# Optimization experiments

Measured on AMD Instinct MI355X. Metric: run time of the kernel, lower is better.

Reference implementation:

```python
import jax, jax.numpy as jnp
import numpy as np

N_NODES, N_EDGES, F_DIM, H_DIM = 50000, 800000, 128, 128
BN_EPS = 1e-3  # keras BatchNormalization default epsilon


def setup_inputs() -> dict:
    key = jax.random.key(0)
    k0, k1, k2 = jax.random.split(key, 3)
    edge_pairs = jax.random.randint(k0, (N_EDGES, 2), 0, N_NODES, dtype=jnp.int64 if jax.config.jax_enable_x64 else jnp.int32)
    node_features = jax.random.normal(k1, (N_NODES, F_DIM), dtype=jnp.float32)
    W = jax.random.normal(k2, (F_DIM, H_DIM), dtype=jnp.float32) * (1.0 / np.sqrt(F_DIM))
    b = jnp.zeros((H_DIM,), jnp.float32)
    gamma = jnp.ones((H_DIM,), jnp.float32)
    beta = jnp.zeros((H_DIM,), jnp.float32)
    moving_mean = jnp.zeros((H_DIM,), jnp.float32)
    moving_var = jnp.ones((H_DIM,), jnp.float32)
    return {"edge_pairs": edge_pairs, "node_features": node_features, "W": W, "b": b,
            "gamma": gamma, "beta": beta, "moving_mean": moving_mean, "moving_var": moving_var}


def reference(edge_pairs, node_features, W, b, gamma, beta, moving_mean, moving_var):
    src = edge_pairs[:, 0]
    dst = edge_pairs[:, 1]
    n = node_features.shape[0]

    # linear transform (dropout inactive: training=False)
    t = node_features @ W + b  # [N, H]

    # out-degree by source node
    deg = jax.ops.segment_sum(jnp.ones(src.shape[0], t.dtype), src, num_segments=n)  # [N]
    inv_sqrt_deg = jnp.power(deg, -0.5)  # matches tf.pow(d, -0.5)

    # degree-normalized neighbour messages: d_src^-1/2 * d_dst^-1/2 * t[dst]
    scale = (inv_sqrt_deg[src] * inv_sqrt_deg[dst])[:, None]  # [E,1]
    nb_sum = jax.ops.segment_sum(t[dst] * scale, src, num_segments=n)  # [N, H]

    # source term: segment_mean(deg[src] * t[src]) ; empty segments -> 0 (tf semantics)
    msg = deg[src][:, None] * t[src]  # [E, H]
    seg = jax.ops.segment_sum(msg, src, num_segments=n)  # [N, H]
    src_mean = jnp.where(deg[:, None] > 0, seg / jnp.maximum(deg, 1.0)[:, None], 0.0)

    agg = 0.5 * nb_sum + 0.5 * src_mean

    # batchnorm, inference mode (moving statistics)
    return (agg - moving_mean) * jax.lax.rsqrt(moving_var + BN_EPS) * gamma + beta
```

## Files before the change

kernel.cpp:

```cpp
#include <hip/hip_runtime.h>
#include <math.h>

#define BN_EPS 0.001f
#define CHUNK 2048
#define MAXBUCK 1024

typedef __attribute__((ext_vector_type(8))) short bf16x8;
typedef __attribute__((ext_vector_type(4))) float f32x4;
typedef __attribute__((ext_vector_type(2))) float f32x2;

__device__ inline unsigned bf16rne(float f) {
  unsigned u = __float_as_uint(f);
  return (u + 0x7fffu + ((u >> 16) & 1u)) >> 16;
}

__global__ __launch_bounds__(256) void k_ehist(const int2* __restrict__ ep, int ne,
                                               int nbuck, int* __restrict__ ghist) {
  __shared__ int h[MAXBUCK];
  int c = blockIdx.x, t = threadIdx.x;
  for (int i = t; i < nbuck; i += 256) h[i] = 0;
  __syncthreads();
  int base = c * CHUNK;
  int end = min(base + CHUNK, ne);
  for (int e = base + t; e < end; e += 256) atomicAdd(&h[ep[e].x >> 6], 1);
  __syncthreads();
  int* row = ghist + (size_t)c * nbuck;
  for (int i = t; i < nbuck; i += 256) row[i] = h[i];
}

__global__ __launch_bounds__(512) void k_bscan(int* __restrict__ ghist, int nchunk,
                                               int nbuck, int* __restrict__ btot) {
  __shared__ int s0[512], s1[512];
  int b = blockIdx.x, t = threadIdx.x;
  int v = (t < nchunk) ? ghist[(size_t)t * nbuck + b] : 0;
  s0[t] = v;
  __syncthreads();
  int* src = s0; int* dst = s1;
  for (int off = 1; off < 512; off <<= 1) {
    int x = src[t];
    if (t >= off) x += src[t - off];
    dst[t] = x;
    __syncthreads();
    int* tmp = src; src = dst; dst = tmp;
  }
  if (t < nchunk) ghist[(size_t)t * nbuck + b] = src[t] - v;
  if (t == 0) btot[b] = src[511];
}

__global__ __launch_bounds__(1024) void k_bbase(const int* __restrict__ btot, int nbuck,
                                                int* __restrict__ bbase) {
  __shared__ int s0[1024], s1[1024];
  int t = threadIdx.x;
  int v = (t < nbuck) ? btot[t] : 0;
  s0[t] = v;
  __syncthreads();
  int* src = s0; int* dst = s1;
  for (int off = 1; off < 1024; off <<= 1) {
    int x = src[t];
    if (t >= off) x += src[t - off];
    dst[t] = x;
    __syncthreads();
    int* tmp = src; src = dst; dst = tmp;
  }
  if (t < nbuck) bbase[t] = src[t] - v;
}

__global__ __launch_bounds__(256) void k_ebin(const int2* __restrict__ ep, int ne,
                                              int nbuck, const int* __restrict__ ghist,
                                              const int* __restrict__ bbase,
                                              unsigned* __restrict__ bins) {
  __shared__ int cur[MAXBUCK];
  int c = blockIdx.x, t = threadIdx.x;
  const int* row = ghist + (size_t)c * nbuck;
  for (int i = t; i < nbuck; i += 256) cur[i] = bbase[i] + row[i];
  __syncthreads();
  int base = c * CHUNK;
  int end = min(base + CHUNK, ne);
  for (int e = base + t; e < end; e += 256) {
    int2 p = ep[e];
    int pos = atomicAdd(&cur[p.x >> 6], 1);
    bins[pos] = (unsigned)p.y | ((unsigned)(p.x & 63) << 17);
  }
}

__global__ __launch_bounds__(256) void k_bfinal(const int* __restrict__ bbase,
                                                const int* __restrict__ btot,
                                                const unsigned* __restrict__ bins,
                                                int n, int* __restrict__ deg,
                                                float* __restrict__ isd,
                                                int* __restrict__ offsets,
                                                int* __restrict__ csr_dst) {
  __shared__ int h[64];
  __shared__ int cur[64];
  int bk = blockIdx.x, t = threadIdx.x;
  if (t < 64) h[t] = 0;
  __syncthreads();
  int s = bbase[bk], cnt = btot[bk];
  for (int i = t; i < cnt; i += 256) atomicAdd(&h[bins[s + i] >> 17], 1);
  __syncthreads();
  if (t == 0) {
    int run = s;
    for (int j = 0; j < 64; ++j) { cur[j] = run; run += h[j]; }
  }
  __syncthreads();
  if (t < 64) {
    int node = (bk << 6) + t;
    if (node < n) {
      deg[node] = h[t];
      offsets[node] = cur[t];
      isd[node] = 1.0f / sqrtf((float)h[t]);
    }
  }
  __syncthreads();
  for (int i = t; i < cnt; i += 256) {
    unsigned r = bins[s + i];
    int pos = atomicAdd(&cur[r >> 17], 1);
    csr_dst[pos] = (int)(r & 0x1FFFFu);
  }
}

__global__ __launch_bounds__(256) void k_wsplit(const float* __restrict__ W,
                                                unsigned short* __restrict__ Wh,
                                                unsigned short* __restrict__ Wl) {
  int g = blockIdx.x * 256 + threadIdx.x;
  int frag = g >> 6;
  int lane = g & 63;
  int ct = frag >> 2, ks = frag & 3;
  int col = ct * 16 + (lane & 15);
  int k0 = ks * 32 + (lane >> 4) * 8;
  unsigned short h8[8], l8[8];
#pragma unroll
  for (int j = 0; j < 8; ++j) {
    float x = W[(size_t)(k0 + j) * 128 + col];
    unsigned short h = (unsigned short)(__float_as_uint(x) >> 16);
    float rem = x - __uint_as_float((unsigned)h << 16);
    h8[j] = h;
    l8[j] = (unsigned short)bf16rne(rem);
  }
  *(uint4*)&Wh[(size_t)frag * 512 + lane * 8] = *(uint4*)h8;
  *(uint4*)&Wl[(size_t)frag * 512 + lane * 8] = *(uint4*)l8;
}

__global__ __launch_bounds__(256, 4) void k_gemm(const float* __restrict__ X,
                                                 const unsigned short* __restrict__ Wh,
                                                 const unsigned short* __restrict__ Wl,
                                                 const float* __restrict__ b,
                                                 const float* __restrict__ isd,
                                                 float* __restrict__ T,
                                                 unsigned char* __restrict__ Tb8, int M) {
  int tid = threadIdx.x;
  int wave = tid >> 6, lane = tid & 63;
  int r16 = lane & 15, kq = lane >> 4;
  int ch = wave & 1;
  int rowbase = blockIdx.x * 32 + (wave >> 1) * 16;
  int arow = rowbase + r16;
  bool aok = arow < M;
  const float* xr = X + ((size_t)arow << 7);

  bf16x8 ah[4], al[4];
#pragma unroll
  for (int ks = 0; ks < 4; ++ks) {
    int k0 = ks * 32 + kq * 8;
    float4 v0 = aok ? *(const float4*)(xr + k0) : make_float4(0.f, 0.f, 0.f, 0.f);
    float4 v1 = aok ? *(const float4*)(xr + k0 + 4) : make_float4(0.f, 0.f, 0.f, 0.f);
    float f[8] = {v0.x, v0.y, v0.z, v0.w, v1.x, v1.y, v1.z, v1.w};
    bf16x8 h8, l8;
#pragma unroll
    for (int j = 0; j < 8; ++j) {
      unsigned short h = (unsigned short)(__float_as_uint(f[j]) >> 16);
      float rem = f[j] - __uint_as_float((unsigned)h << 16);
      h8[j] = (short)h;
      l8[j] = (short)bf16rne(rem);
    }
    ah[ks] = h8;
    al[ks] = l8;
  }

  f32x4 acc[4] = {};
#pragma unroll
  for (int ks = 0; ks < 4; ++ks) {
#pragma unroll
    for (int ct = 0; ct < 4; ++ct) {
      int frag = (ch * 4 + ct) * 4 + ks;
      bf16x8 bh = *(const bf16x8*)&Wh[(size_t)frag * 512 + lane * 8];
      bf16x8 bl = *(const bf16x8*)&Wl[(size_t)frag * 512 + lane * 8];
      acc[ct] = __builtin_amdgcn_mfma_f32_16x16x32_bf16(ah[ks], bh, acc[ct], 0, 0, 0);
      acc[ct] = __builtin_amdgcn_mfma_f32_16x16x32_bf16(ah[ks], bl, acc[ct], 0, 0, 0);
      acc[ct] = __builtin_amdgcn_mfma_f32_16x16x32_bf16(al[ks], bh, acc[ct], 0, 0, 0);
    }
  }

  float bias[4];
#pragma unroll
  for (int ct = 0; ct < 4; ++ct) bias[ct] = b[(ch * 4 + ct) * 16 + r16];
  int orow[4];
  float isdr[4];
#pragma unroll
  for (int r = 0; r < 4; ++r) {
    orow[r] = rowbase + kq * 4 + r;
    isdr[r] = (orow[r] < M) ? isd[orow[r]] : 0.f;
  }
#pragma unroll
  for (int ct = 0; ct < 4; ++ct) {
    int col = (ch * 4 + ct) * 16 + r16;
#pragma unroll
    for (int r = 0; r < 4; ++r) {
      float v = acc[ct][r] + bias[ct];
      bool ok = orow[r] < M;
      if (ok) T[((size_t)orow[r] << 7) + col] = v;
      float sv = v * isdr[r];
      float other = __shfl_xor(sv, 1);
      int pk01 = __builtin_amdgcn_cvt_pk_fp8_f32(sv, other, 0, false);
      int pk23 = __shfl_xor(pk01, 2);
      if (ok && (r16 & 3) == 0) {
        unsigned dword = ((unsigned)pk01 & 0xFFFFu) | ((unsigned)pk23 << 16);
        *(unsigned*)&Tb8[((size_t)orow[r] << 7) + (ch * 4 + ct) * 16 + r16] = dword;
      }
    }
  }
}

__global__ __launch_bounds__(256) void k_gather(
    const float* __restrict__ T, const unsigned char* __restrict__ Tb8,
    const int* __restrict__ deg, const float* __restrict__ isd,
    const int* __restrict__ offsets, const int* __restrict__ csr_dst,
    const float* __restrict__ mm, const float* __restrict__ var,
    const float* __restrict__ gamma, const float* __restrict__ beta,
    float* __restrict__ out, int n, int ne) {
  int wave = threadIdx.x >> 6;
  int lane = threadIdx.x & 63;
  int i = blockIdx.x * 4 + wave;
  if (i >= n) return;
  int degi = deg[i];
  int start = offsets[i];
  const unsigned short* rows = (const unsigned short*)Tb8;
  float sx[16] = {}, sy[16] = {};
  for (int e = 0; e < degi; e += 16) {
    int ii = start + e + (lane & 15);
    int dv = (ii < ne) ? csr_dst[ii] : 0;
    unsigned short r[16];
#pragma unroll
    for (int j = 0; j < 16; ++j) {
      int idx = __shfl(dv, j);
      r[j] = rows[((size_t)idx << 6) + lane];
    }
#pragma unroll
    for (int j = 0; j < 16; ++j) {
      int rr = (e + j < degi) ? (int)r[j] : 0;
      f32x2 f = __builtin_amdgcn_cvt_pk_f32_fp8(rr, false);
      sx[j] += f.x;
      sy[j] += f.y;
    }
  }
  float fx = (((sx[0] + sx[1]) + (sx[2] + sx[3])) + ((sx[4] + sx[5]) + (sx[6] + sx[7]))) +
             (((sx[8] + sx[9]) + (sx[10] + sx[11])) + ((sx[12] + sx[13]) + (sx[14] + sx[15])));
  float fy = (((sy[0] + sy[1]) + (sy[2] + sy[3])) + ((sy[4] + sy[5]) + (sy[6] + sy[7]))) +
             (((sy[8] + sy[9]) + (sy[10] + sy[11])) + ((sy[12] + sy[13]) + (sy[14] + sy[15])));
  float aggx = 0.f, aggy = 0.f;
  if (degi > 0) {
    float2 tv = ((const float2*)(T + ((size_t)i << 7)))[lane];
    float isi = isd[i];
    float di = (float)degi;
    aggx = 0.5f * (isi * fx) + 0.5f * (di * tv.x);
    aggy = 0.5f * (isi * fy) + 0.5f * (di * tv.y);
  }
  float2 mmv = ((const float2*)mm)[lane];
  float2 vv = ((const float2*)var)[lane];
  float2 gv = ((const float2*)gamma)[lane];
  float2 bv = ((const float2*)beta)[lane];
  float2 res;
  res.x = (aggx - mmv.x) * rsqrtf(vv.x + BN_EPS) * gv.x + bv.x;
  res.y = (aggy - mmv.y) * rsqrtf(vv.y + BN_EPS) * gv.y + bv.y;
  ((float2*)(out + ((size_t)i << 7)))[lane] = res;
}

static inline size_t align_up(size_t x) { return (x + 255) & ~(size_t)255; }

extern "C" void kernel_launch(void* const* d_in, const int* in_sizes, int n_in,
                              void* d_out, int out_size, void* d_ws, size_t ws_size,
                              hipStream_t stream) {
  const int2* ep = (const int2*)d_in[0];
  const float* X = (const float*)d_in[1];
  const float* W = (const float*)d_in[2];
  const float* b = (const float*)d_in[3];
  const float* gamma = (const float*)d_in[4];
  const float* beta = (const float*)d_in[5];
  const float* mm = (const float*)d_in[6];
  const float* var = (const float*)d_in[7];
  float* out = (float*)d_out;

  const int ne = in_sizes[0] / 2;
  const int n = in_sizes[1] / 128;
  const int nbuck = (n + 63) >> 6;
  const int nchunk = (ne + CHUNK - 1) / CHUNK;

  char* p = (char*)d_ws;
  int* deg = (int*)p;        p += align_up((size_t)n * 4);
  float* isd = (float*)p;    p += align_up((size_t)n * 4);
  int* offsets = (int*)p;    p += align_up((size_t)n * 4);
  int* btot = (int*)p;       p += align_up((size_t)nbuck * 4);
  int* bbase = (int*)p;      p += align_up((size_t)nbuck * 4);
  int* ghist = (int*)p;      p += align_up((size_t)nchunk * nbuck * 4);
  int* csr_dst = (int*)p;    p += align_up((size_t)ne * 4);
  unsigned* bins = (unsigned*)p; p += align_up((size_t)ne * 4);
  unsigned short* Wh = (unsigned short*)p; p += align_up((size_t)128 * 128 * 2);
  unsigned short* Wl = (unsigned short*)p; p += align_up((size_t)128 * 128 * 2);
  float* T = (float*)p;      p += align_up((size_t)n * 128 * 4);
  unsigned char* Tb8 = (unsigned char*)p; p += align_up((size_t)n * 128);

  k_ehist<<<nchunk, 256, 0, stream>>>(ep, ne, nbuck, ghist);
  k_bscan<<<nbuck, 512, 0, stream>>>(ghist, nchunk, nbuck, btot);
  k_bbase<<<1, 1024, 0, stream>>>(btot, nbuck, bbase);
  k_ebin<<<nchunk, 256, 0, stream>>>(ep, ne, nbuck, ghist, bbase, bins);
  k_bfinal<<<nbuck, 256, 0, stream>>>(bbase, btot, bins, n, deg, isd, offsets, csr_dst);
  k_wsplit<<<8, 256, 0, stream>>>(W, Wh, Wl);
  k_gemm<<<(n + 31) / 32, 256, 0, stream>>>(X, Wh, Wl, b, isd, T, Tb8, n);
  k_gather<<<(n + 3) / 4, 256, 0, stream>>>(T, Tb8, deg, isd, offsets, csr_dst,
                                            mm, var, gamma, beta, out, n, ne);
}
```

Measured before the change: 96.13 us.

## Double GEMM row tile per wave, enlarge edge chunks, simplify fp8 store

Each GEMM wave now computes two 16-row tiles, so every W fragment load is reused across 32 rows, and the block covers 64 rows with occupancy lowered to 3. The edge-binning chunk size is doubled, halving the chunk count so the bucket scan runs with 256 threads. The fp8 side-output is written as one byte per lane instead of shuffle-packed dwords. The weight-split launch is moved first. Byte stores may coalesce less well and the higher register use may reduce occupancy.

```diff
diff --git a/kernel.cpp b/kernel.cpp
--- a/kernel.cpp
+++ b/kernel.cpp
@@ -2,7 +2,7 @@
 #include <math.h>
 
 #define BN_EPS 0.001f
-#define CHUNK 2048
+#define CHUNK 4096
 #define MAXBUCK 1024
 
 typedef __attribute__((ext_vector_type(8))) short bf16x8;
@@ -28,15 +28,15 @@
   for (int i = t; i < nbuck; i += 256) row[i] = h[i];
 }
 
-__global__ __launch_bounds__(512) void k_bscan(int* __restrict__ ghist, int nchunk,
+__global__ __launch_bounds__(256) void k_bscan(int* __restrict__ ghist, int nchunk,
                                                int nbuck, int* __restrict__ btot) {
-  __shared__ int s0[512], s1[512];
+  __shared__ int s0[256], s1[256];
   int b = blockIdx.x, t = threadIdx.x;
   int v = (t < nchunk) ? ghist[(size_t)t * nbuck + b] : 0;
   s0[t] = v;
   __syncthreads();
   int* src = s0; int* dst = s1;
-  for (int off = 1; off < 512; off <<= 1) {
+  for (int off = 1; off < 256; off <<= 1) {
     int x = src[t];
     if (t >= off) x += src[t - off];
     dst[t] = x;
@@ -44,7 +44,7 @@
     int* tmp = src; src = dst; dst = tmp;
   }
   if (t < nchunk) ghist[(size_t)t * nbuck + b] = src[t] - v;
-  if (t == 0) btot[b] = src[511];
+  if (t == 0) btot[b] = src[255];
 }
 
 __global__ __launch_bounds__(1024) void k_bbase(const int* __restrict__ btot, int nbuck,
@@ -141,7 +141,7 @@
   *(uint4*)&Wl[(size_t)frag * 512 + lane * 8] = *(uint4*)l8;
 }
 
-__global__ __launch_bounds__(256, 4) void k_gemm(const float* __restrict__ X,
+__global__ __launch_bounds__(256, 3) void k_gemm(const float* __restrict__ X,
                                                  const unsigned short* __restrict__ Wh,
                                                  const unsigned short* __restrict__ Wl,
                                                  const float* __restrict__ b,
@@ -152,31 +152,34 @@
   int wave = tid >> 6, lane = tid & 63;
   int r16 = lane & 15, kq = lane >> 4;
   int ch = wave & 1;
-  int rowbase = blockIdx.x * 32 + (wave >> 1) * 16;
-  int arow = rowbase + r16;
-  bool aok = arow < M;
-  const float* xr = X + ((size_t)arow << 7);
-
-  bf16x8 ah[4], al[4];
-#pragma unroll
-  for (int ks = 0; ks < 4; ++ks) {
-    int k0 = ks * 32 + kq * 8;
-    float4 v0 = aok ? *(const float4*)(xr + k0) : make_float4(0.f, 0.f, 0.f, 0.f);
-    float4 v1 = aok ? *(const float4*)(xr + k0 + 4) : make_float4(0.f, 0.f, 0.f, 0.f);
-    float f[8] = {v0.x, v0.y, v0.z, v0.w, v1.x, v1.y, v1.z, v1.w};
-    bf16x8 h8, l8;
-#pragma unroll
-    for (int j = 0; j < 8; ++j) {
-      unsigned short h = (unsigned short)(__float_as_uint(f[j]) >> 16);
-      float rem = f[j] - __uint_as_float((unsigned)h << 16);
-      h8[j] = (short)h;
-      l8[j] = (short)bf16rne(rem);
-    }
-    ah[ks] = h8;
-    al[ks] = l8;
-  }
-
-  f32x4 acc[4] = {};
+  int rowbase = blockIdx.x * 64 + (wave >> 1) * 32;
+
+  bf16x8 ah[2][4], al[2][4];
+#pragma unroll
+  for (int rt = 0; rt < 2; ++rt) {
+    int row = rowbase + rt * 16 + r16;
+    bool ok = row < M;
+    const float* xr = X + ((size_t)row << 7);
+#pragma unroll
+    for (int ks = 0; ks < 4; ++ks) {
+      int k0 = ks * 32 + kq * 8;
+      float4 v0 = ok ? *(const float4*)(xr + k0) : make_float4(0.f, 0.f, 0.f, 0.f);
+      float4 v1 = ok ? *(const float4*)(xr + k0 + 4) : make_float4(0.f, 0.f, 0.f, 0.f);
+      float f[8] = {v0.x, v0.y, v0.z, v0.w, v1.x, v1.y, v1.z, v1.w};
+      bf16x8 h8, l8;
+#pragma unroll
+      for (int j = 0; j < 8; ++j) {
+        unsigned short h = (unsigned short)(__float_as_uint(f[j]) >> 16);
+        float rem = f[j] - __uint_as_float((unsigned)h << 16);
+        h8[j] = (short)h;
+        l8[j] = (short)bf16rne(rem);
+      }
+      ah[rt][ks] = h8;
+      al[rt][ks] = l8;
+    }
+  }
+
+  f32x4 acc[2][4] = {};
 #pragma unroll
   for (int ks = 0; ks < 4; ++ks) {
 #pragma unroll
@@ -184,37 +187,39 @@
       int frag = (ch * 4 + ct) * 4 + ks;
       bf16x8 bh = *(const bf16x8*)&Wh[(size_t)frag * 512 + lane * 8];
       bf16x8 bl = *(const bf16x8*)&Wl[(size_t)frag * 512 + lane * 8];
-      acc[ct] = __builtin_amdgcn_mfma_f32_16x16x32_bf16(ah[ks], bh, acc[ct], 0, 0, 0);
-      acc[ct] = __builtin_amdgcn_mfma_f32_16x16x32_bf16(ah[ks], bl, acc[ct], 0, 0, 0);
-      acc[ct] = __builtin_amdgcn_mfma_f32_16x16x32_bf16(al[ks], bh, acc[ct], 0, 0, 0);
+#pragma unroll
+      for (int rt = 0; rt < 2; ++rt) {
+        acc[rt][ct] = __builtin_amdgcn_mfma_f32_16x16x32_bf16(ah[rt][ks], bh, acc[rt][ct], 0, 0, 0);
+        acc[rt][ct] = __builtin_amdgcn_mfma_f32_16x16x32_bf16(ah[rt][ks], bl, acc[rt][ct], 0, 0, 0);
+        acc[rt][ct] = __builtin_amdgcn_mfma_f32_16x16x32_bf16(al[rt][ks], bh, acc[rt][ct], 0, 0, 0);
+      }
     }
   }
 
   float bias[4];
 #pragma unroll
   for (int ct = 0; ct < 4; ++ct) bias[ct] = b[(ch * 4 + ct) * 16 + r16];
-  int orow[4];
-  float isdr[4];
-#pragma unroll
-  for (int r = 0; r < 4; ++r) {
-    orow[r] = rowbase + kq * 4 + r;
-    isdr[r] = (orow[r] < M) ? isd[orow[r]] : 0.f;
-  }
-#pragma unroll
-  for (int ct = 0; ct < 4; ++ct) {
-    int col = (ch * 4 + ct) * 16 + r16;
+#pragma unroll
+  for (int rt = 0; rt < 2; ++rt) {
+    int orow[4];
+    float isdr[4];
 #pragma unroll
     for (int r = 0; r < 4; ++r) {
-      float v = acc[ct][r] + bias[ct];
-      bool ok = orow[r] < M;
-      if (ok) T[((size_t)orow[r] << 7) + col] = v;
-      float sv = v * isdr[r];
-      float other = __shfl_xor(sv, 1);
-      int pk01 = __builtin_amdgcn_cvt_pk_fp8_f32(sv, other, 0, false);
-      int pk23 = __shfl_xor(pk01, 2);
-      if (ok && (r16 & 3) == 0) {
-        unsigned dword = ((unsigned)pk01 & 0xFFFFu) | ((unsigned)pk23 << 16);
-        *(unsigned*)&Tb8[((size_t)orow[r] << 7) + (ch * 4 + ct) * 16 + r16] = dword;
+      orow[r] = rowbase + rt * 16 + kq * 4 + r;
+      isdr[r] = (orow[r] < M) ? isd[orow[r]] : 0.f;
+    }
+#pragma unroll
+    for (int ct = 0; ct < 4; ++ct) {
+      int col = (ch * 4 + ct) * 16 + r16;
+#pragma unroll
+      for (int r = 0; r < 4; ++r) {
+        float v = acc[rt][ct][r] + bias[ct];
+        if (orow[r] < M) {
+          T[((size_t)orow[r] << 7) + col] = v;
+          float sv = v * isdr[r];
+          int pk = __builtin_amdgcn_cvt_pk_fp8_f32(sv, sv, 0, false);
+          Tb8[((size_t)orow[r] << 7) + col] = (unsigned char)pk;
+        }
       }
     }
   }
@@ -308,13 +313,13 @@
   float* T = (float*)p;      p += align_up((size_t)n * 128 * 4);
   unsigned char* Tb8 = (unsigned char*)p; p += align_up((size_t)n * 128);
 
+  k_wsplit<<<8, 256, 0, stream>>>(W, Wh, Wl);
   k_ehist<<<nchunk, 256, 0, stream>>>(ep, ne, nbuck, ghist);
-  k_bscan<<<nbuck, 512, 0, stream>>>(ghist, nchunk, nbuck, btot);
+  k_bscan<<<nbuck, 256, 0, stream>>>(ghist, nchunk, nbuck, btot);
   k_bbase<<<1, 1024, 0, stream>>>(btot, nbuck, bbase);
   k_ebin<<<nchunk, 256, 0, stream>>>(ep, ne, nbuck, ghist, bbase, bins);
   k_bfinal<<<nbuck, 256, 0, stream>>>(bbase, btot, bins, n, deg, isd, offsets, csr_dst);
-  k_wsplit<<<8, 256, 0, stream>>>(W, Wh, Wl);
-  k_gemm<<<(n + 31) / 32, 256, 0, stream>>>(X, Wh, Wl, b, isd, T, Tb8, n);
+  k_gemm<<<(n + 63) / 64, 256, 0, stream>>>(X, Wh, Wl, b, isd, T, Tb8, n);
   k_gather<<<(n + 3) / 4, 256, 0, stream>>>(T, Tb8, deg, isd, offsets, csr_dst,
                                             mm, var, gamma, beta, out, n, ne);
 }
```

New measurement: 102.8 us. +6.9%, slower.
